# Performance work log

Measured on AMD Instinct MI355X. Metric: run time of the kernel, lower is better.

The kernel has to match this reference:

```python
import jax, jax.numpy as jnp
import numpy as np

K = 2
BN_EPS = 1e-5


def setup_inputs() -> dict:
    key = jax.random.key(0)
    k1, k2, k3 = jax.random.split(key, 3)
    B, C, H, W, D, O = 4, 128, 32, 32, 32, 128
    x = jax.random.normal(k1, (B, C, H, W, D), dtype=jnp.float32)
    conv_w = jax.random.normal(k2, (O, 2 * C), dtype=jnp.float32) * 0.02  # 1x1x1 conv kernel
    conv_b = jax.random.normal(k3, (O,), dtype=jnp.float32) * 0.02
    bn_gamma = jnp.ones((O,), dtype=jnp.float32)
    bn_beta = jnp.zeros((O,), dtype=jnp.float32)
    return {"x": x, "conv_w": conv_w, "conv_b": conv_b,
            "bn_gamma": bn_gamma, "bn_beta": bn_beta}


def _axis_running_max(x, x_j, axis, dim):
    # torch.cat([x[..., -i:], x[..., :-i]], axis) == jnp.roll(x, i, axis)
    shifts = jnp.arange(K, dim, K)

    def step(carry, s):
        diff = x - jnp.roll(x, s, axis=axis)
        return jnp.maximum(carry, diff), None

    x_j, _ = jax.lax.scan(step, x_j, shifts)
    return x_j


def reference(x, conv_w, conv_b, bn_gamma, bn_beta):
    B, C, H, W, D = x.shape
    x_j = jnp.zeros_like(x)
    x_j = _axis_running_max(x, x_j, 2, H)
    x_j = _axis_running_max(x, x_j, 3, W)
    x_j = _axis_running_max(x, x_j, 4, D)
    x_j = jax.lax.stop_gradient(x_j)  # original detaches every x_j update

    xc = jnp.concatenate([x, x_j], axis=1)  # [B, 2C, H, W, D]
    # 1x1x1 Conv3d == per-voxel channel GEMM
    y = jnp.einsum('bchwd,oc->bohwd', xc, conv_w) + conv_b[None, :, None, None, None]

    # BatchNorm3d, training mode (batch statistics over B,H,W,D)
    mean = y.mean(axis=(0, 2, 3, 4), keepdims=True)
    var = ((y - mean) ** 2).mean(axis=(0, 2, 3, 4), keepdims=True)
    yn = (y - mean) * jax.lax.rsqrt(var + BN_EPS)
    yn = yn * bn_gamma[None, :, None, None, None] + bn_beta[None, :, None, None, None]

    # torch nn.GELU default is exact erf form
    return jax.nn.gelu(yn, approximate=False)
```

## Files before the change

### kernel.cpp

```cpp
#include <hip/hip_runtime.h>
#include <hip/hip_bf16.h>

#define BB 4
#define CCH 128
#define C2 256
#define OO 128
#define NVOX 32768
#define NTOT (BB*NVOX)

typedef __attribute__((ext_vector_type(4))) float f32x4;
typedef __attribute__((ext_vector_type(8))) short s16x8;
typedef __attribute__((ext_vector_type(4))) unsigned int u32x4;
typedef __attribute__((ext_vector_type(2))) unsigned int u32x2;
typedef unsigned int u32;
typedef unsigned short u16;

#define SWZ(r) ((((r)>>3) ^ (r)) & 7)

__device__ __forceinline__ float bf2f(short s){
  union { u32 i; float f; } cv; cv.i = ((u32)(u16)s) << 16; return cv.f;
}
__device__ __forceinline__ short f2bf(float f){
  union { __hip_bfloat16 h; short s; } cv; cv.h = __float2bfloat16(f); return cv.s;
}
__device__ __forceinline__ u32 pack2(float a, float b){
  return ((u32)(u16)f2bf(a)) | (((u32)(u16)f2bf(b)) << 16);
}
__device__ __forceinline__ float ulo(u32 r){
  union { u32 i; float f; } cv; cv.i = r << 16; return cv.f;
}
__device__ __forceinline__ float uhi(u32 r){
  union { u32 i; float f; } cv; cv.i = r & 0xffff0000u; return cv.f;
}
__device__ __forceinline__ float bfr(float f){ return bf2f(f2bf(f)); }

__global__ __launch_bounds__(256) void k_convw(const float* __restrict__ w, short* __restrict__ wb){
  int i = blockIdx.x*256 + threadIdx.x;
  wb[i] = f2bf(w[i]);
}

__global__ __launch_bounds__(1024) void k_tab(const float* __restrict__ x,
                                              u32* __restrict__ tw, u32* __restrict__ th,
                                              u32* __restrict__ td){
  int t = threadIdx.x;
  u32 bc = blockIdx.x;
  const float* __restrict__ src = x + (size_t)bc*NVOX;
  int a = t >> 5, d = t & 31;
  {
    float m1[2] = {1e30f,1e30f}, m2[2] = {1e30f,1e30f};
    #pragma unroll
    for(int w=0;w<32;w++){
      float v = bfr(src[a*1024 + w*32 + d]);
      int p = w & 1;
      m2[p] = fminf(m2[p], fmaxf(m1[p], v));
      m1[p] = fminf(m1[p], v);
    }
    u32* r = tw + (size_t)bc*2048 + a*64;
    r[d]      = pack2(m1[0], m2[0]);
    r[32 + d] = pack2(m1[1], m2[1]);
  }
  {
    float m1[2] = {1e30f,1e30f}, m2[2] = {1e30f,1e30f};
    #pragma unroll
    for(int h=0;h<32;h++){
      float v = bfr(src[h*1024 + a*32 + d]);
      int p = h & 1;
      m2[p] = fminf(m2[p], fmaxf(m1[p], v));
      m1[p] = fminf(m1[p], v);
    }
    u32* r = th + (size_t)bc*2048 + a*32;
    r[d]        = pack2(m1[0], m2[0]);
    r[1024 + d] = pack2(m1[1], m2[1]);
  }
  {
    const float* pl = src + t*32;
    f32x4 v[8];
    #pragma unroll
    for(int g=0;g<8;g++) v[g] = *(const f32x4*)(pl + g*4);
    float m1[2]={1e30f,1e30f}, m2[2]={1e30f,1e30f};
    #pragma unroll
    for(int g=0;g<8;g++){
      #pragma unroll
      for(int i=0;i<4;i++){
        float r = bfr(v[g][i]);
        int p = i & 1;
        m2[p] = fminf(m2[p], fmaxf(m1[p], r));
        m1[p] = fminf(m1[p], r);
      }
    }
    *(u32x2*)(td + (size_t)bc*2048 + t*2) = (u32x2){pack2(m1[0],m2[0]), pack2(m1[1],m2[1])};
  }
}

__global__ __launch_bounds__(256) void k_gemm(const float* __restrict__ x, const short* __restrict__ wb,
                                              const u32* __restrict__ tw, const u32* __restrict__ th,
                                              const u32* __restrict__ td,
                                              short* __restrict__ y, float* __restrict__ part){
  __shared__ __align__(16) char lds[65536];
  char* ldsJ = lds + 32768;
  u32 blk = blockIdx.x;
  u32 vblk = blk & 255, b = blk >> 8;
  u32 vbase = vblk * 128;
  const float* __restrict__ xb = x + (size_t)b*CCH*NVOX + vbase;
  int t = threadIdx.x;
  int wave = t >> 6, lane = t & 63;
  int wr = wave >> 1, wc = wave & 1;
  int l15 = lane & 15, l4 = lane >> 4;

  {
    int v0   = (t & 15) * 8;
    int line = (t & 15) >> 2;
    int d0   = (t & 3) * 8;
    int cb2  = 2 * (t >> 4);
    int h  = vbase >> 10;
    int w  = ((vbase >> 5) & 31) + line;
    int lidx = h*32 + w;
    #pragma unroll
    for(int g=0;g<2;g++){
      f32x4 xe0[2], xe1[2], xo0[2], xo1[2];
      u32x4 we0[2], we1[2], wo0[2], wo1[2];
      u32x4 he0[2], he1[2], ho0[2], ho1[2];
      u32x2 tde[2], tdo[2];
      #pragma unroll
      for(int u=0;u<2;u++){
        int c = cb2 + 64*g + 32*u;
        const float* pe = xb + (size_t)c*NVOX + v0;
        const float* po = pe + NVOX;
        xe0[u] = *(const f32x4*)(pe);     xe1[u] = *(const f32x4*)(pe + 4);
        xo0[u] = *(const f32x4*)(po);     xo1[u] = *(const f32x4*)(po + 4);
        size_t bce = ((size_t)b*CCH + c)*2048;
        const u32* twE = tw + bce + h*64 + (w&1)*32 + d0;
        const u32* thE = th + bce + (h&1)*1024 + w*32 + d0;
        we0[u] = *(const u32x4*)(twE);        we1[u] = *(const u32x4*)(twE + 4);
        wo0[u] = *(const u32x4*)(twE + 2048); wo1[u] = *(const u32x4*)(twE + 2052);
        he0[u] = *(const u32x4*)(thE);        he1[u] = *(const u32x4*)(thE + 4);
        ho0[u] = *(const u32x4*)(thE + 2048); ho1[u] = *(const u32x4*)(thE + 2052);
        const u32* tdE = td + bce + lidx*2;
        tde[u] = *(const u32x2*)(tdE);
        tdo[u] = *(const u32x2*)(tdE + 2048);
      }
      #pragma unroll
      for(int u=0;u<2;u++){
        int c = cb2 + 64*g + 32*u;
        u32 pr[8];
        #pragma unroll
        for(int e=0;e<4;e++){
          pr[e]   = pack2(xe0[u][e], xo0[u][e]);
          pr[4+e] = pack2(xe1[u][e], xo1[u][e]);
        }
        #pragma unroll
        for(int e=0;e<8;e++){
          int v = v0 + e;
          *(u32*)(lds + v*256 + ((((c>>3) ^ SWZ(v))<<4) | ((c&7)<<1))) = pr[e];
        }
        float dm1e[2] = {ulo(tde[u][0]), ulo(tde[u][1])};
        float dm2e[2] = {uhi(tde[u][0]), uhi(tde[u][1])};
        float dm1o[2] = {ulo(tdo[u][0]), ulo(tdo[u][1])};
        float dm2o[2] = {uhi(tdo[u][0]), uhi(tdo[u][1])};
        #pragma unroll
        for(int e=0;e<8;e++){
          int p = e & 1;
          float xe = ulo(pr[e]), xo = uhi(pr[e]);
          u32 wE = (e<4) ? we0[u][e] : we1[u][e-4];
          u32 wO = (e<4) ? wo0[u][e] : wo1[u][e-4];
          u32 hE = (e<4) ? he0[u][e] : he1[u][e-4];
          u32 hO = (e<4) ? ho0[u][e] : ho1[u][e-4];
          float mDe = (xe == dm1e[p]) ? dm2e[p] : dm1e[p];
          float mDo = (xo == dm1o[p]) ? dm2o[p] : dm1o[p];
          float w1e = ulo(wE); float mWe = (xe == w1e) ? uhi(wE) : w1e;
          float w1o = ulo(wO); float mWo = (xo == w1o) ? uhi(wO) : w1o;
          float h1e = ulo(hE); float mHe = (xe == h1e) ? uhi(hE) : h1e;
          float h1o = ulo(hO); float mHo = (xo == h1o) ? uhi(hO) : h1o;
          float je = fmaxf(0.f, xe - fminf(mDe, fminf(mWe, mHe)));
          float jo = fmaxf(0.f, xo - fminf(mDo, fminf(mWo, mHo)));
          int v = v0 + e;
          *(u32*)(ldsJ + v*256 + ((((c>>3) ^ SWZ(v))<<4) | ((c&7)<<1))) = pack2(je, jo);
        }
      }
    }
  }
  __syncthreads();

  f32x4 acc[4][4];
  #pragma unroll
  for(int mt=0;mt<4;mt++)
    #pragma unroll
    for(int nt=0;nt<4;nt++) acc[mt][nt] = (f32x4){0.f,0.f,0.f,0.f};
  #pragma unroll
  for(int kc=0;kc<2;kc++){
    const char* tile = (kc == 0) ? lds : ldsJ;
    #pragma unroll
    for(int ks=0;ks<4;ks++){
      int kk = ks*32 + l4*8;
      s16x8 afrag[4], bfrag[4];
      #pragma unroll
      for(int nt=0;nt<4;nt++){
        int vloc = wc*64 + nt*16 + l15;
        bfrag[nt] = *(const s16x8*)(tile + vloc*256 + (((kk>>3) ^ SWZ(vloc))<<4));
      }
      #pragma unroll
      for(int mt=0;mt<4;mt++){
        int o = wr*64 + mt*16 + l15;
        afrag[mt] = *(const s16x8*)(wb + o*C2 + kc*128 + kk);
      }
      #pragma unroll
      for(int mt=0;mt<4;mt++)
        #pragma unroll
        for(int nt=0;nt<4;nt++)
          acc[mt][nt] = __builtin_amdgcn_mfma_f32_16x16x32_bf16(afrag[mt], bfrag[nt], acc[mt][nt], 0,0,0);
    }
  }

  __syncthreads();
  #pragma unroll
  for(int mt=0;mt<4;mt++){
    #pragma unroll
    for(int nt=0;nt<4;nt++){
      int vcol = wc*64 + nt*16 + l15;
      #pragma unroll
      for(int r=0;r<4;r++){
        int o = wr*64 + mt*16 + l4*4 + r;
        *(short*)(lds + o*256 + ((((vcol>>3) ^ SWZ(o))<<4) | ((vcol&7)<<1))) = f2bf(acc[mt][nt][r]);
      }
    }
  }
  __syncthreads();
  short* __restrict__ yb = y + (size_t)b*OO*NVOX + vbase;
  #pragma unroll
  for(int q=0;q<8;q++){
    int p = t + q*256;
    int o = p >> 4, vs = (p & 15) * 8;
    s16x8 val = *(const s16x8*)(lds + o*256 + ((((vs>>3) ^ SWZ(o))<<4)));
    *(s16x8*)(yb + (size_t)o*NVOX + vs) = val;
  }

  {
    int o = t >> 1, vh = t & 1;
    float sm = 0.f, ss = 0.f;
    #pragma unroll
    for(int k=0;k<8;k++){
      int vs = vh*64 + k*8;
      s16x8 val = *(const s16x8*)(lds + o*256 + ((((vs>>3) ^ SWZ(o))<<4)));
      #pragma unroll
      for(int e=0;e<8;e++){ float f = bf2f(val[e]); sm += f; ss += f*f; }
    }
    sm += __shfl_xor(sm, 1);
    ss += __shfl_xor(ss, 1);
    if(vh == 0){
      float* pp = part + ((size_t)blk*OO + o)*2;
      pp[0] = sm; pp[1] = ss;
    }
  }
}

__global__ __launch_bounds__(256) void k_statsf(const float* __restrict__ part, float* __restrict__ stats){
  int o = blockIdx.x, t = threadIdx.x;
  float sm = 0.f, ss = 0.f;
  #pragma unroll
  for(int k=0;k<4;k++){
    int blk = t + k*256;
    const float* pp = part + ((size_t)blk*OO + o)*2;
    sm += pp[0]; ss += pp[1];
  }
  __shared__ float rs[256], rss[256];
  rs[t] = sm; rss[t] = ss;
  __syncthreads();
  for(int k=128;k>0;k>>=1){
    if(t<k){ rs[t]+=rs[t+k]; rss[t]+=rss[t+k]; }
    __syncthreads();
  }
  if(t==0){
    float inv = 1.0f/(float)NTOT;
    float mean = rs[0]*inv;
    float var = rss[0]*inv - mean*mean;
    stats[2*o]   = mean;
    stats[2*o+1] = rsqrtf(var + 1e-5f);
  }
}

__global__ __launch_bounds__(256) void k_bngelu(const short* __restrict__ y, const float* __restrict__ stats,
                                                const float* __restrict__ gamma, const float* __restrict__ beta,
                                                float* __restrict__ out){
  size_t base = ((size_t)blockIdx.x*256 + threadIdx.x)*8;
  int o = (int)((base >> 15) & 127);
  float mean = stats[2*o], rstd = stats[2*o+1];
  float g  = gamma[o]*rstd;
  float be = beta[o] - mean*g;
  s16x8 u = *(const s16x8*)(y + base);
  f32x4 r0, r1;
  #pragma unroll
  for(int e=0;e<8;e++){
    float yn = bf2f(u[e])*g + be;
    float ge = 0.5f*yn*(1.0f + erff(yn*0.70710678118654752f));
    if(e<4) r0[e] = ge; else r1[e-4] = ge;
  }
  *(f32x4*)(out + base)     = r0;
  *(f32x4*)(out + base + 4) = r1;
}

extern "C" void kernel_launch(void* const* d_in, const int* in_sizes, int n_in,
                              void* d_out, int out_size, void* d_ws, size_t ws_size,
                              hipStream_t stream) {
  (void)in_sizes; (void)n_in; (void)out_size; (void)ws_size;
  const float* x     = (const float*)d_in[0];
  const float* cw    = (const float*)d_in[1];
  const float* gamma = (const float*)d_in[3];
  const float* beta  = (const float*)d_in[4];
  float* out = (float*)d_out;

  char* ws = (char*)d_ws;
  short* wb    = (short*)ws;
  short* y     = (short*)(ws + 65536);
  float* stats = (float*)(ws + 65536 + (size_t)BB*OO*NVOX*2);
  float* part  = stats + 256;
  u32* tw = (u32*)d_out;
  u32* th = tw + (size_t)512*2048;
  u32* td = th + (size_t)512*2048;

  k_convw <<<dim3((OO*C2)/256),     dim3(256), 0, stream>>>(cw, wb);
  k_tab   <<<dim3(BB*CCH),         dim3(1024), 0, stream>>>(x, tw, th, td);
  k_gemm  <<<dim3(BB*(NVOX/128)),  dim3(256), 0, stream>>>(x, wb, tw, th, td, y, part);
  k_statsf<<<dim3(OO),             dim3(256), 0, stream>>>(part, stats);
  k_bngelu<<<dim3((NTOT*OO)/2048), dim3(256), 0, stream>>>(y, stats, gamma, beta, out);
}
```

Baseline: 95.07 us.

## Process two voxel tiles per GEMM block and prefetch next tile's x during MFMA

Each k_gemm block now handles two consecutive 128-voxel tiles, halving the grid to 512 blocks. The x loads for the second tile are issued right after the first tile's LDS fill, so they can overlap the first tile's MFMA loop and epilogue. This aims to hide global load latency and cut per-block launch overhead. In exchange it holds 16 extra f32x4 registers per thread, which may lower occupancy, and gives fewer blocks for the 256 CUs to share. A stray __syncthreads was also added in k_statsf.

```diff
diff --git a/kernel.cpp b/kernel.cpp
--- a/kernel.cpp
+++ b/kernel.cpp
@@ -99,157 +99,171 @@
   __shared__ __align__(16) char lds[65536];
   char* ldsJ = lds + 32768;
   u32 blk = blockIdx.x;
-  u32 vblk = blk & 255, b = blk >> 8;
-  u32 vbase = vblk * 128;
-  const float* __restrict__ xb = x + (size_t)b*CCH*NVOX + vbase;
+  u32 pairidx = blk & 127, b = blk >> 7;
+  u32 vb0 = pairidx * 256;
+  const float* __restrict__ xb = x + (size_t)b*CCH*NVOX;
   int t = threadIdx.x;
   int wave = t >> 6, lane = t & 63;
   int wr = wave >> 1, wc = wave & 1;
   int l15 = lane & 15, l4 = lane >> 4;
-
-  {
-    int v0   = (t & 15) * 8;
-    int line = (t & 15) >> 2;
-    int d0   = (t & 3) * 8;
-    int cb2  = 2 * (t >> 4);
-    int h  = vbase >> 10;
-    int w  = ((vbase >> 5) & 31) + line;
+  int v0   = (t & 15) * 8;
+  int line = (t & 15) >> 2;
+  int d0   = (t & 3) * 8;
+  int cb2  = 2 * (t >> 4);
+
+  f32x4 px[16];
+  #pragma unroll
+  for(int gu=0; gu<4; ++gu){
+    int c = cb2 + 32*gu;
+    const float* pe = xb + (size_t)c*NVOX + vb0 + v0;
+    px[gu*4+0] = *(const f32x4*)(pe);
+    px[gu*4+1] = *(const f32x4*)(pe + 4);
+    px[gu*4+2] = *(const f32x4*)(pe + NVOX);
+    px[gu*4+3] = *(const f32x4*)(pe + NVOX + 4);
+  }
+
+  #pragma unroll
+  for(int it=0; it<2; ++it){
+    u32 vbase = vb0 + it*128;
+    int h = vbase >> 10;
+    int w = ((vbase >> 5) & 31) + line;
     int lidx = h*32 + w;
-    #pragma unroll
-    for(int g=0;g<2;g++){
-      f32x4 xe0[2], xe1[2], xo0[2], xo1[2];
-      u32x4 we0[2], we1[2], wo0[2], wo1[2];
-      u32x4 he0[2], he1[2], ho0[2], ho1[2];
-      u32x2 tde[2], tdo[2];
-      #pragma unroll
-      for(int u=0;u<2;u++){
-        int c = cb2 + 64*g + 32*u;
-        const float* pe = xb + (size_t)c*NVOX + v0;
-        const float* po = pe + NVOX;
-        xe0[u] = *(const f32x4*)(pe);     xe1[u] = *(const f32x4*)(pe + 4);
-        xo0[u] = *(const f32x4*)(po);     xo1[u] = *(const f32x4*)(po + 4);
-        size_t bce = ((size_t)b*CCH + c)*2048;
-        const u32* twE = tw + bce + h*64 + (w&1)*32 + d0;
-        const u32* thE = th + bce + (h&1)*1024 + w*32 + d0;
-        we0[u] = *(const u32x4*)(twE);        we1[u] = *(const u32x4*)(twE + 4);
-        wo0[u] = *(const u32x4*)(twE + 2048); wo1[u] = *(const u32x4*)(twE + 2052);
-        he0[u] = *(const u32x4*)(thE);        he1[u] = *(const u32x4*)(thE + 4);
-        ho0[u] = *(const u32x4*)(thE + 2048); ho1[u] = *(const u32x4*)(thE + 2052);
-        const u32* tdE = td + bce + lidx*2;
-        tde[u] = *(const u32x2*)(tdE);
-        tdo[u] = *(const u32x2*)(tdE + 2048);
-      }
-      #pragma unroll
-      for(int u=0;u<2;u++){
-        int c = cb2 + 64*g + 32*u;
-        u32 pr[8];
-        #pragma unroll
-        for(int e=0;e<4;e++){
-          pr[e]   = pack2(xe0[u][e], xo0[u][e]);
-          pr[4+e] = pack2(xe1[u][e], xo1[u][e]);
+
+    #pragma unroll
+    for(int gu=0; gu<4; ++gu){
+      int c = cb2 + 32*gu;
+      size_t bce = ((size_t)b*CCH + c)*2048;
+      const u32* twE = tw + bce + h*64 + (w&1)*32 + d0;
+      const u32* thE = th + bce + (h&1)*1024 + w*32 + d0;
+      u32x4 we0 = *(const u32x4*)(twE),        we1 = *(const u32x4*)(twE + 4);
+      u32x4 wo0 = *(const u32x4*)(twE + 2048), wo1 = *(const u32x4*)(twE + 2052);
+      u32x4 he0 = *(const u32x4*)(thE),        he1 = *(const u32x4*)(thE + 4);
+      u32x4 ho0 = *(const u32x4*)(thE + 2048), ho1 = *(const u32x4*)(thE + 2052);
+      const u32* tdE = td + bce + lidx*2;
+      u32x2 tde = *(const u32x2*)(tdE);
+      u32x2 tdo = *(const u32x2*)(tdE + 2048);
+      f32x4 xe0 = px[gu*4+0], xe1 = px[gu*4+1];
+      f32x4 xo0 = px[gu*4+2], xo1 = px[gu*4+3];
+      u32 pr[8];
+      #pragma unroll
+      for(int e=0;e<4;e++){
+        pr[e]   = pack2(xe0[e], xo0[e]);
+        pr[4+e] = pack2(xe1[e], xo1[e]);
+      }
+      #pragma unroll
+      for(int e=0;e<8;e++){
+        int v = v0 + e;
+        *(u32*)(lds + v*256 + ((((c>>3) ^ SWZ(v))<<4) | ((c&7)<<1))) = pr[e];
+      }
+      float dm1e[2] = {ulo(tde[0]), ulo(tde[1])};
+      float dm2e[2] = {uhi(tde[0]), uhi(tde[1])};
+      float dm1o[2] = {ulo(tdo[0]), ulo(tdo[1])};
+      float dm2o[2] = {uhi(tdo[0]), uhi(tdo[1])};
+      #pragma unroll
+      for(int e=0;e<8;e++){
+        int p = e & 1;
+        float xe = ulo(pr[e]), xo = uhi(pr[e]);
+        u32 wE = (e<4) ? we0[e] : we1[e-4];
+        u32 wO = (e<4) ? wo0[e] : wo1[e-4];
+        u32 hE = (e<4) ? he0[e] : he1[e-4];
+        u32 hO = (e<4) ? ho0[e] : ho1[e-4];
+        float mDe = (xe == dm1e[p]) ? dm2e[p] : dm1e[p];
+        float mDo = (xo == dm1o[p]) ? dm2o[p] : dm1o[p];
+        float w1e = ulo(wE); float mWe = (xe == w1e) ? uhi(wE) : w1e;
+        float w1o = ulo(wO); float mWo = (xo == w1o) ? uhi(wO) : w1o;
+        float h1e = ulo(hE); float mHe = (xe == h1e) ? uhi(hE) : h1e;
+        float h1o = ulo(hO); float mHo = (xo == h1o) ? uhi(hO) : h1o;
+        float je = fmaxf(0.f, xe - fminf(mDe, fminf(mWe, mHe)));
+        float jo = fmaxf(0.f, xo - fminf(mDo, fminf(mWo, mHo)));
+        int v = v0 + e;
+        *(u32*)(ldsJ + v*256 + ((((c>>3) ^ SWZ(v))<<4) | ((c&7)<<1))) = pack2(je, jo);
+      }
+    }
+    __syncthreads();
+
+    if(it == 0){
+      #pragma unroll
+      for(int gu=0; gu<4; ++gu){
+        int c = cb2 + 32*gu;
+        const float* pe = xb + (size_t)c*NVOX + vb0 + 128 + v0;
+        px[gu*4+0] = *(const f32x4*)(pe);
+        px[gu*4+1] = *(const f32x4*)(pe + 4);
+        px[gu*4+2] = *(const f32x4*)(pe + NVOX);
+        px[gu*4+3] = *(const f32x4*)(pe + NVOX + 4);
+      }
+    }
+
+    f32x4 acc[4][4];
+    #pragma unroll
+    for(int mt=0;mt<4;mt++)
+      #pragma unroll
+      for(int nt=0;nt<4;nt++) acc[mt][nt] = (f32x4){0.f,0.f,0.f,0.f};
+    #pragma unroll
+    for(int kc=0;kc<2;kc++){
+      const char* tile = (kc == 0) ? lds : ldsJ;
+      #pragma unroll
+      for(int ks=0;ks<4;ks++){
+        int kk = ks*32 + l4*8;
+        s16x8 afrag[4], bfrag[4];
+        #pragma unroll
+        for(int nt=0;nt<4;nt++){
+          int vloc = wc*64 + nt*16 + l15;
+          bfrag[nt] = *(const s16x8*)(tile + vloc*256 + (((kk>>3) ^ SWZ(vloc))<<4));
         }
         #pragma unroll
-        for(int e=0;e<8;e++){
-          int v = v0 + e;
-          *(u32*)(lds + v*256 + ((((c>>3) ^ SWZ(v))<<4) | ((c&7)<<1))) = pr[e];
+        for(int mt=0;mt<4;mt++){
+          int o = wr*64 + mt*16 + l15;
+          afrag[mt] = *(const s16x8*)(wb + o*C2 + kc*128 + kk);
         }
-        float dm1e[2] = {ulo(tde[u][0]), ulo(tde[u][1])};
-        float dm2e[2] = {uhi(tde[u][0]), uhi(tde[u][1])};
-        float dm1o[2] = {ulo(tdo[u][0]), ulo(tdo[u][1])};
-        float dm2o[2] = {uhi(tdo[u][0]), uhi(tdo[u][1])};
-        #pragma unroll
-        for(int e=0;e<8;e++){
-          int p = e & 1;
-          float xe = ulo(pr[e]), xo = uhi(pr[e]);
-          u32 wE = (e<4) ? we0[u][e] : we1[u][e-4];
-          u32 wO = (e<4) ? wo0[u][e] : wo1[u][e-4];
-          u32 hE = (e<4) ? he0[u][e] : he1[u][e-4];
-          u32 hO = (e<4) ? ho0[u][e] : ho1[u][e-4];
-          float mDe = (xe == dm1e[p]) ? dm2e[p] : dm1e[p];
-          float mDo = (xo == dm1o[p]) ? dm2o[p] : dm1o[p];
-          float w1e = ulo(wE); float mWe = (xe == w1e) ? uhi(wE) : w1e;
-          float w1o = ulo(wO); float mWo = (xo == w1o) ? uhi(wO) : w1o;
-          float h1e = ulo(hE); float mHe = (xe == h1e) ? uhi(hE) : h1e;
-          float h1o = ulo(hO); float mHo = (xo == h1o) ? uhi(hO) : h1o;
-          float je = fmaxf(0.f, xe - fminf(mDe, fminf(mWe, mHe)));
-          float jo = fmaxf(0.f, xo - fminf(mDo, fminf(mWo, mHo)));
-          int v = v0 + e;
-          *(u32*)(ldsJ + v*256 + ((((c>>3) ^ SWZ(v))<<4) | ((c&7)<<1))) = pack2(je, jo);
+        #pragma unroll
+        for(int mt=0;mt<4;mt++)
+          #pragma unroll
+          for(int nt=0;nt<4;nt++)
+            acc[mt][nt] = __builtin_amdgcn_mfma_f32_16x16x32_bf16(afrag[mt], bfrag[nt], acc[mt][nt], 0,0,0);
+      }
+    }
+
+    __syncthreads();
+    #pragma unroll
+    for(int mt=0;mt<4;mt++){
+      #pragma unroll
+      for(int nt=0;nt<4;nt++){
+        int vcol = wc*64 + nt*16 + l15;
+        #pragma unroll
+        for(int r=0;r<4;r++){
+          int o = wr*64 + mt*16 + l4*4 + r;
+          *(short*)(lds + o*256 + ((((vcol>>3) ^ SWZ(o))<<4) | ((vcol&7)<<1))) = f2bf(acc[mt][nt][r]);
         }
       }
     }
-  }
-  __syncthreads();
-
-  f32x4 acc[4][4];
-  #pragma unroll
-  for(int mt=0;mt<4;mt++)
-    #pragma unroll
-    for(int nt=0;nt<4;nt++) acc[mt][nt] = (f32x4){0.f,0.f,0.f,0.f};
-  #pragma unroll
-  for(int kc=0;kc<2;kc++){
-    const char* tile = (kc == 0) ? lds : ldsJ;
-    #pragma unroll
-    for(int ks=0;ks<4;ks++){
-      int kk = ks*32 + l4*8;
-      s16x8 afrag[4], bfrag[4];
-      #pragma unroll
-      for(int nt=0;nt<4;nt++){
-        int vloc = wc*64 + nt*16 + l15;
-        bfrag[nt] = *(const s16x8*)(tile + vloc*256 + (((kk>>3) ^ SWZ(vloc))<<4));
-      }
-      #pragma unroll
-      for(int mt=0;mt<4;mt++){
-        int o = wr*64 + mt*16 + l15;
-        afrag[mt] = *(const s16x8*)(wb + o*C2 + kc*128 + kk);
-      }
-      #pragma unroll
-      for(int mt=0;mt<4;mt++)
-        #pragma unroll
-        for(int nt=0;nt<4;nt++)
-          acc[mt][nt] = __builtin_amdgcn_mfma_f32_16x16x32_bf16(afrag[mt], bfrag[nt], acc[mt][nt], 0,0,0);
-    }
-  }
-
-  __syncthreads();
-  #pragma unroll
-  for(int mt=0;mt<4;mt++){
-    #pragma unroll
-    for(int nt=0;nt<4;nt++){
-      int vcol = wc*64 + nt*16 + l15;
-      #pragma unroll
-      for(int r=0;r<4;r++){
-        int o = wr*64 + mt*16 + l4*4 + r;
-        *(short*)(lds + o*256 + ((((vcol>>3) ^ SWZ(o))<<4) | ((vcol&7)<<1))) = f2bf(acc[mt][nt][r]);
-      }
-    }
-  }
-  __syncthreads();
-  short* __restrict__ yb = y + (size_t)b*OO*NVOX + vbase;
-  #pragma unroll
-  for(int q=0;q<8;q++){
-    int p = t + q*256;
-    int o = p >> 4, vs = (p & 15) * 8;
-    s16x8 val = *(const s16x8*)(lds + o*256 + ((((vs>>3) ^ SWZ(o))<<4)));
-    *(s16x8*)(yb + (size_t)o*NVOX + vs) = val;
-  }
-
-  {
-    int o = t >> 1, vh = t & 1;
-    float sm = 0.f, ss = 0.f;
-    #pragma unroll
-    for(int k=0;k<8;k++){
-      int vs = vh*64 + k*8;
+    __syncthreads();
+    short* __restrict__ yb = y + (size_t)b*OO*NVOX + vbase;
+    #pragma unroll
+    for(int q=0;q<8;q++){
+      int p = t + q*256;
+      int o = p >> 4, vs = (p & 15) * 8;
       s16x8 val = *(const s16x8*)(lds + o*256 + ((((vs>>3) ^ SWZ(o))<<4)));
-      #pragma unroll
-      for(int e=0;e<8;e++){ float f = bf2f(val[e]); sm += f; ss += f*f; }
-    }
-    sm += __shfl_xor(sm, 1);
-    ss += __shfl_xor(ss, 1);
-    if(vh == 0){
-      float* pp = part + ((size_t)blk*OO + o)*2;
-      pp[0] = sm; pp[1] = ss;
-    }
+      *(s16x8*)(yb + (size_t)o*NVOX + vs) = val;
+    }
+    {
+      u32 blk_t = b*256 + pairidx*2 + it;
+      int o = t >> 1, vh = t & 1;
+      float sm = 0.f, ss = 0.f;
+      #pragma unroll
+      for(int k=0;k<8;k++){
+        int vs = vh*64 + k*8;
+        s16x8 val = *(const s16x8*)(lds + o*256 + ((((vs>>3) ^ SWZ(o))<<4)));
+        #pragma unroll
+        for(int e=0;e<8;e++){ float f = bf2f(val[e]); sm += f; ss += f*f; }
+      }
+      sm += __shfl_xor(sm, 1);
+      ss += __shfl_xor(ss, 1);
+      if(vh == 0){
+        float* pp = part + ((size_t)blk_t*OO + o)*2;
+        pp[0] = sm; pp[1] = ss;
+      }
+    }
+    if(it == 0) __syncthreads();
   }
 }
 
@@ -263,6 +277,7 @@
     sm += pp[0]; ss += pp[1];
   }
   __shared__ float rs[256], rss[256];
+  __syncthreads();
   rs[t] = sm; rss[t] = ss;
   __syncthreads();
   for(int k=128;k>0;k>>=1){
@@ -319,7 +334,7 @@
 
   k_convw <<<dim3((OO*C2)/256),     dim3(256), 0, stream>>>(cw, wb);
   k_tab   <<<dim3(BB*CCH),         dim3(1024), 0, stream>>>(x, tw, th, td);
-  k_gemm  <<<dim3(BB*(NVOX/128)),  dim3(256), 0, stream>>>(x, wb, tw, th, td, y, part);
+  k_gemm  <<<dim3(512),            dim3(256), 0, stream>>>(x, wb, tw, th, td, y, part);
   k_statsf<<<dim3(OO),             dim3(256), 0, stream>>>(part, stats);
   k_bngelu<<<dim3((NTOT*OO)/2048), dim3(256), 0, stream>>>(y, stats, gamma, beta, out);
 }
```

New measurement: 118.8 us. +25.0%, slower.
